# Optimization experiments

Measured on AMD Instinct MI355X. Metric: run time of the kernel, lower is better.

## Reference

```python
import jax, jax.numpy as jnp
import numpy as np

B, C, HIM, WIM = 128, 3, 224, 224
P = 14                      # num_patches per side
PATCH = HIM // P            # 16
IN_D = C * PATCH * PATCH    # 768
D = 256                     # hidden_dim
H = 8                       # num_heads
DH = D // H                 # 32
L = 4                       # num_blocks
OUT = 1000
S = P * P + 1               # 197 tokens incl. class token
EPS = 1e-5


def make_patches(images):
    n, c, h, w = images.shape
    ph, pw = h // P, w // P
    x = images.reshape(n, c, P, ph, P, pw)
    x = x.transpose(0, 2, 4, 1, 3, 5)          # (n, P, P, c, ph, pw)
    return x.reshape(n, P * P, c * ph * pw)


def positional_encodings():
    pos = jnp.arange(S, dtype=jnp.float32)[:, None]
    j = jnp.arange(D)[None, :]
    angle = pos / jnp.power(10000.0, (2 * (j // 2)).astype(jnp.float32) / D)
    return jnp.where(j % 2 == 0, jnp.sin(angle), jnp.cos(angle))  # (S, D)


def layernorm(x, g, b):
    mu = jnp.mean(x, axis=-1, keepdims=True)
    var = jnp.mean(jnp.square(x - mu), axis=-1, keepdims=True)
    return (x - mu) / jnp.sqrt(var + EPS) * g + b


def setup_inputs() -> dict:
    key = jax.random.key(0)
    ks = jax.random.split(key, 32)
    r = lambda k, shp: jax.random.normal(k, shp, jnp.float32) * 0.02
    inp = {
        "images": jax.random.normal(ks[0], (B, C, HIM, WIM), jnp.float32),
        "w_map": r(ks[1], (D, IN_D)), "b_map": r(ks[2], (D,)),
        "cls_tok": jax.random.uniform(ks[3], (1, D), jnp.float32),
        "norm1_g": jnp.ones((L, D)), "norm1_b": jnp.zeros((L, D)),
        "wq": r(ks[4], (L, H, DH, DH)), "bq": r(ks[5], (L, H, DH)),
        "wk": r(ks[6], (L, H, DH, DH)), "bk": r(ks[7], (L, H, DH)),
        "wv": r(ks[8], (L, H, DH, DH)), "bv": r(ks[9], (L, H, DH)),
        "w_last": r(ks[10], (L, D, D)), "b_last": r(ks[11], (L, D)),
        "norm2_g": jnp.ones((L, D)), "norm2_b": jnp.zeros((L, D)),
        "w_mlp1": r(ks[12], (L, 4 * D, D)), "b_mlp1": r(ks[13], (L, 4 * D)),
        "w_mlp2": r(ks[14], (L, D, 4 * D)), "b_mlp2": r(ks[15], (L, D)),
        "w_out": r(ks[16], (OUT, D)), "b_out": r(ks[17], (OUT,)),
    }
    return inp


def reference(images, w_map, b_map, cls_tok, norm1_g, norm1_b,
              wq, bq, wk, bk, wv, bv, w_last, b_last,
              norm2_g, norm2_b, w_mlp1, b_mlp1, w_mlp2, b_mlp2,
              w_out, b_out):
    n = images.shape[0]
    patches = make_patches(images)                         # (n, P*P, IN_D)
    tokens = jnp.einsum('npi,di->npd', patches, w_map) + b_map
    cls = jnp.broadcast_to(cls_tok[None], (n, 1, D))
    out = jnp.concatenate([cls, tokens], axis=1) + positional_encodings()[None]
    scale = 1.0 / jnp.sqrt(jnp.float32(DH))
    for l in range(L):
        x1 = layernorm(out, norm1_g[l], norm1_b[l])
        xh = x1.reshape(n, S, H, DH)
        # per-head Linear: y = x @ W^T + b (torch convention W[out,in])
        q = jnp.einsum('nshd,hed->nshe', xh, wq[l]) + bq[l]
        k = jnp.einsum('nshd,hed->nshe', xh, wk[l]) + bk[l]
        v = jnp.einsum('nshd,hed->nshe', xh, wv[l]) + bv[l]
        attn = jax.nn.softmax(jnp.einsum('nshd,nthd->nhst', q, k) * scale, axis=-1)
        o = jnp.einsum('nhst,nthd->nshd', attn, v).reshape(n, S, D)
        o = jnp.einsum('nsd,ed->nse', o, w_last[l]) + b_last[l]
        out = out + o
        x2 = layernorm(out, norm2_g[l], norm2_b[l])
        h1 = jax.nn.gelu(jnp.einsum('nsd,fd->nsf', x2, w_mlp1[l]) + b_mlp1[l],
                         approximate=False)
        out = out + jnp.einsum('nsf,df->nsd', h1, w_mlp2[l]) + b_mlp2[l]
    cls_out = out[:, 0]                                    # (n, D)
    logits = cls_out @ w_out.T + b_out                     # (n, OUT)
    return jax.nn.softmax(logits, axis=1)
```

## Files before the change

kernel.cpp:

```cpp
#include <hip/hip_runtime.h>
#include <hip/hip_bf16.h>
#include <math.h>


#define SEQ 197
#define DIM 256
#define NB  128
#define MROWS (NB * SEQ)

typedef __attribute__((ext_vector_type(4))) float f32x4;
typedef __attribute__((ext_vector_type(8))) __bf16 bf16x8;
typedef __attribute__((ext_vector_type(8))) short s16x8;

#define GLOAD16(g, l)                                                          \
    __builtin_amdgcn_global_load_lds(                                          \
        (const __attribute__((address_space(1))) void*)(g),                    \
        (__attribute__((address_space(3))) void*)(l), 16, 0, 0)

__device__ __forceinline__ unsigned bf16_rn(float x) {
    union { float f; unsigned u; } c; c.f = x;
    return (c.u + 0x7fffu + ((c.u >> 16) & 1u)) >> 16;
}
__device__ __forceinline__ void split2(float a, unsigned short& hi, unsigned short& lo) {
    unsigned h = bf16_rn(a);
    hi = (unsigned short)h;
    union { unsigned u; float f; } hf; hf.u = h << 16;
    lo = (unsigned short)bf16_rn(a - hf.f);
}
__device__ __forceinline__ int swz(int row, int c) {
    return row * 32 + ((c ^ ((row >> 1) & 3)) << 3);
}

__global__ __launch_bounds__(256) void pe_kernel(float* __restrict__ pe) {
    int s = blockIdx.x, j = threadIdx.x;
    int jh = j >> 1;
    float expo = (float)(2 * jh) * (1.0f / 256.0f);
    float inv_freq = exp2f(-expo * 13.287712379549449f);
    float angle = (float)s * inv_freq;
    pe[s * 256 + j] = (j & 1) ? cosf(angle) : sinf(angle);
}

__global__ __launch_bounds__(256) void embed_cls(const float* __restrict__ cls_tok,
                                                 const float* __restrict__ pe,
                                                 float* __restrict__ out) {
    int n = blockIdx.x, d = threadIdx.x;
    out[(size_t)n * SEQ * DIM + d] = cls_tok[d] + pe[d];
}

__global__ __launch_bounds__(256) void split_weights(const float* __restrict__ src,
                                                     unsigned short* __restrict__ hi,
                                                     unsigned short* __restrict__ lo, int n) {
    for (int i = blockIdx.x * 256 + threadIdx.x; i < n; i += gridDim.x * 256) {
        unsigned short h, l;
        split2(src[i], h, l);
        hi[i] = h; lo[i] = l;
    }
}

__global__ __launch_bounds__(256) void pack_qkv_c(const float* __restrict__ wq,
                                                  const float* __restrict__ wk,
                                                  const float* __restrict__ wv,
                                                  unsigned short* __restrict__ wc) {
    int e = blockIdx.x * 256 + threadIdx.x;
    if (e >= 98304) return;
    int l = e / 24576, r = e % 24576;
    int j = r >> 5, d = r & 31;
    int m = j >> 8, hh = (j >> 5) & 7, ee = j & 31;
    const float* w = (m == 0) ? wq : (m == 1) ? wk : wv;
    wc[e] = (unsigned short)bf16_rn(w[(((size_t)l * 8 + hh) * 32 + ee) * 32 + d]);
}

__global__ __launch_bounds__(256) void pack_qkv_b(const float* __restrict__ bq,
                                                  const float* __restrict__ bk,
                                                  const float* __restrict__ bv,
                                                  float* __restrict__ bp) {
    int e = blockIdx.x * 256 + threadIdx.x;
    if (e >= 3072) return;
    int l = e / 768, j = e % 768;
    int m = j >> 8, jj = j & 255;
    const float* b = (m == 0) ? bq : (m == 1) ? bk : bv;
    bp[e] = b[l * 256 + jj];
}

template <int ACT, int OMODE, bool ALO>
__global__ __launch_bounds__(256) void gemm_as(const unsigned short* __restrict__ Ahi,
                                               const unsigned short* __restrict__ Alo,
                                               const unsigned short* __restrict__ Bhi,
                                               const unsigned short* __restrict__ Blo,
                                               const float* __restrict__ bias,
                                               float* __restrict__ C,
                                               unsigned short* __restrict__ Chi,
                                               unsigned short* __restrict__ Clo,
                                               int M, int N, int K) {
    __shared__ unsigned short Ah[4096], Al[4096], Bh[4096], Bl[4096];
    const int tid = threadIdx.x;
    const int bm = blockIdx.y * 128, bn = blockIdx.x * 128;
    const int lane = tid & 63, wid = tid >> 6;
    const int wm = wid & 1, wn = wid >> 1;
    const int q = lane >> 4, r15 = lane & 15;
    const int rl = lane >> 2, cc = lane & 3;
    const int wr = wid * 32;

    const int row0 = wr + rl, row1 = wr + 16 + rl;
    const int cx0 = (cc ^ ((row0 >> 1) & 3)) << 3;
    const int cx1 = (cc ^ ((row1 >> 1) & 3)) << 3;
    const unsigned short* ah0 = Ahi + (size_t)(bm + row0) * K + cx0;
    const unsigned short* ah1 = Ahi + (size_t)(bm + row1) * K + cx1;
    const unsigned short* al0 = Alo + (size_t)(bm + row0) * K + cx0;
    const unsigned short* al1 = Alo + (size_t)(bm + row1) * K + cx1;
    const unsigned short* bh0 = Bhi + (size_t)(bn + row0) * K + cx0;
    const unsigned short* bh1 = Bhi + (size_t)(bn + row1) * K + cx1;
    const unsigned short* bl0 = Blo + (size_t)(bn + row0) * K + cx0;
    const unsigned short* bl1 = Blo + (size_t)(bn + row1) * K + cx1;

    f32x4 acc[4][4];
#pragma unroll
    for (int i = 0; i < 4; ++i)
#pragma unroll
        for (int j = 0; j < 4; ++j) acc[i][j] = (f32x4){0.f, 0.f, 0.f, 0.f};

    for (int k0 = 0; k0 < K; k0 += 32) {
        GLOAD16(ah0 + k0, &Ah[wr * 32]);
        GLOAD16(ah1 + k0, &Ah[(wr + 16) * 32]);
        if constexpr (ALO) {
            GLOAD16(al0 + k0, &Al[wr * 32]);
            GLOAD16(al1 + k0, &Al[(wr + 16) * 32]);
        }
        GLOAD16(bh0 + k0, &Bh[wr * 32]);
        GLOAD16(bh1 + k0, &Bh[(wr + 16) * 32]);
        GLOAD16(bl0 + k0, &Bl[wr * 32]);
        GLOAD16(bl1 + k0, &Bl[(wr + 16) * 32]);
        __syncthreads();

        s16x8 ah[4], al[4], bhf[4], blf[4];
#pragma unroll
        for (int m = 0; m < 4; ++m) {
            int row = wm * 64 + m * 16 + r15;
            int off = row * 32 + ((q ^ ((row >> 1) & 3)) << 3);
            ah[m] = *(const s16x8*)&Ah[off];
            if constexpr (ALO) al[m] = *(const s16x8*)&Al[off];
        }
#pragma unroll
        for (int n = 0; n < 4; ++n) {
            int row = wn * 64 + n * 16 + r15;
            int off = row * 32 + ((q ^ ((row >> 1) & 3)) << 3);
            bhf[n] = *(const s16x8*)&Bh[off];
            blf[n] = *(const s16x8*)&Bl[off];
        }
#pragma unroll
        for (int m = 0; m < 4; ++m)
#pragma unroll
            for (int n = 0; n < 4; ++n) {
                bf16x8 a_h = __builtin_bit_cast(bf16x8, ah[m]);
                bf16x8 b_h = __builtin_bit_cast(bf16x8, bhf[n]);
                bf16x8 b_l = __builtin_bit_cast(bf16x8, blf[n]);
                acc[m][n] = __builtin_amdgcn_mfma_f32_16x16x32_bf16(a_h, b_h, acc[m][n], 0, 0, 0);
                acc[m][n] = __builtin_amdgcn_mfma_f32_16x16x32_bf16(a_h, b_l, acc[m][n], 0, 0, 0);
                if constexpr (ALO) {
                    bf16x8 a_l = __builtin_bit_cast(bf16x8, al[m]);
                    acc[m][n] = __builtin_amdgcn_mfma_f32_16x16x32_bf16(a_l, b_h, acc[m][n], 0, 0, 0);
                }
            }
        __syncthreads();
    }

#pragma unroll
    for (int n = 0; n < 4; ++n) {
        int col = bn + wn * 64 + n * 16 + r15;
        float bb = bias[col];
#pragma unroll
        for (int m = 0; m < 4; ++m) {
            int r0 = bm + wm * 64 + m * 16 + q * 4;
#pragma unroll
            for (int i = 0; i < 4; ++i) {
                float v = acc[m][n][i] + bb;
                if (ACT == 1) v = 0.5f * v * (1.0f + erff(v * 0.70710678118654752f));
                size_t off = (size_t)(r0 + i) * N + col;
                if constexpr (OMODE == 0) C[off] = v;
                else if constexpr (OMODE == 1) C[off] += v;
                else if constexpr (OMODE == 2) {
                    unsigned short hh, ll; split2(v, hh, ll);
                    Chi[off] = hh; Clo[off] = ll;
                } else {
                    Chi[off] = (unsigned short)bf16_rn(v);
                }
            }
        }
    }
}

__global__ __launch_bounds__(256) void gemm_qkv2(const unsigned short* __restrict__ Ahi,
                                                 const unsigned short* __restrict__ Alo,
                                                 const unsigned short* __restrict__ Bc,
                                                 const float* __restrict__ bias,
                                                 unsigned short* __restrict__ Chi,
                                                 unsigned short* __restrict__ Clo) {
    __shared__ unsigned short Ah[4096], Al[4096], Bh[4096];
    const int tid = threadIdx.x;
    const int bm = blockIdx.y * 128, bn = blockIdx.x * 128;
    const int lane = tid & 63, wid = tid >> 6;
    const int wm = wid & 1, wn = wid >> 1;
    const int q = lane >> 4, r15 = lane & 15;
    const int rl = lane >> 2, cc = lane & 3;
    const int wr = wid * 32;
    const int K = 256, N = 768;

    const int row0 = wr + rl, row1 = wr + 16 + rl;
    const int cx0 = (cc ^ ((row0 >> 1) & 3)) << 3;
    const int cx1 = (cc ^ ((row1 >> 1) & 3)) << 3;
    const unsigned short* ah0 = Ahi + (size_t)(bm + row0) * K + cx0;
    const unsigned short* ah1 = Ahi + (size_t)(bm + row1) * K + cx1;
    const unsigned short* al0 = Alo + (size_t)(bm + row0) * K + cx0;
    const unsigned short* al1 = Alo + (size_t)(bm + row1) * K + cx1;

    const int srow = tid >> 2, sc = tid & 3;
    const int j0 = bn + srow, j1 = bn + srow + 64;
    const int c0 = (j0 >> 5) & 7, c1 = (j1 >> 5) & 7;
    const unsigned short* bc0 = Bc + (size_t)j0 * 32 + sc * 8;
    const unsigned short* bc1 = Bc + (size_t)j1 * 32 + sc * 8;
    const int soff0 = swz(srow, sc), soff1 = swz(srow + 64, sc);

    f32x4 acc[4][4];
#pragma unroll
    for (int i = 0; i < 4; ++i)
#pragma unroll
        for (int j = 0; j < 4; ++j) acc[i][j] = (f32x4){0.f, 0.f, 0.f, 0.f};

    const s16x8 bz = (s16x8){0, 0, 0, 0, 0, 0, 0, 0};
    for (int k0 = 0; k0 < K; k0 += 32) {
        const int kc = k0 >> 5;
        GLOAD16(ah0 + k0, &Ah[wr * 32]);
        GLOAD16(ah1 + k0, &Ah[(wr + 16) * 32]);
        GLOAD16(al0 + k0, &Al[wr * 32]);
        GLOAD16(al1 + k0, &Al[(wr + 16) * 32]);
        *(s16x8*)&Bh[soff0] = (c0 == kc) ? *(const s16x8*)bc0 : bz;
        *(s16x8*)&Bh[soff1] = (c1 == kc) ? *(const s16x8*)bc1 : bz;
        __syncthreads();

        s16x8 ah[4], al[4], bhf[4];
#pragma unroll
        for (int m = 0; m < 4; ++m) {
            int row = wm * 64 + m * 16 + r15;
            int off = row * 32 + ((q ^ ((row >> 1) & 3)) << 3);
            ah[m] = *(const s16x8*)&Ah[off];
            al[m] = *(const s16x8*)&Al[off];
        }
#pragma unroll
        for (int n = 0; n < 4; ++n) {
            int row = wn * 64 + n * 16 + r15;
            int off = row * 32 + ((q ^ ((row >> 1) & 3)) << 3);
            bhf[n] = *(const s16x8*)&Bh[off];
        }
#pragma unroll
        for (int m = 0; m < 4; ++m)
#pragma unroll
            for (int n = 0; n < 4; ++n) {
                bf16x8 a_h = __builtin_bit_cast(bf16x8, ah[m]);
                bf16x8 a_l = __builtin_bit_cast(bf16x8, al[m]);
                bf16x8 b_h = __builtin_bit_cast(bf16x8, bhf[n]);
                acc[m][n] = __builtin_amdgcn_mfma_f32_16x16x32_bf16(a_h, b_h, acc[m][n], 0, 0, 0);
                acc[m][n] = __builtin_amdgcn_mfma_f32_16x16x32_bf16(a_l, b_h, acc[m][n], 0, 0, 0);
            }
        __syncthreads();
    }

#pragma unroll
    for (int n = 0; n < 4; ++n) {
        int col = bn + wn * 64 + n * 16 + r15;
        float bb = bias[col];
#pragma unroll
        for (int m = 0; m < 4; ++m) {
            int r0 = bm + wm * 64 + m * 16 + q * 4;
#pragma unroll
            for (int i = 0; i < 4; ++i) {
                float v = acc[m][n][i] + bb;
                size_t off = (size_t)(r0 + i) * N + col;
                unsigned short hh, ll; split2(v, hh, ll);
                Chi[off] = hh; Clo[off] = ll;
            }
        }
    }
}

__global__ __launch_bounds__(256) void patch_mfma(const float* __restrict__ images,
                                                  const unsigned short* __restrict__ Bhi,
                                                  const unsigned short* __restrict__ Blo,
                                                  const float* __restrict__ b_map,
                                                  const float* __restrict__ pe,
                                                  float* __restrict__ out) {
    __shared__ unsigned short Ah[4096], Al[4096], Bh[4096], Bl[4096];
    const int tid = threadIdx.x;
    const int bm = blockIdx.y * 128, bn = blockIdx.x * 128;
    const int lane = tid & 63, wid = tid >> 6;
    const int wm = wid & 1, wn = wid >> 1;
    const int q = lane >> 4, r15 = lane & 15;
    const int srow = tid >> 2, sc = tid & 3;

    const float* ibase[2];
    {
        int rows[2] = {bm + srow, bm + srow + 64};
#pragma unroll
        for (int t = 0; t < 2; ++t) {
            int n = rows[t] / 196, p = rows[t] % 196;
            ibase[t] = images + (size_t)n * 150528 + (size_t)(p / 14) * 3584 + (p % 14) * 16;
        }
    }
    const int soff0 = swz(srow, sc), soff1 = swz(srow + 64, sc);
    const unsigned short* bh0 = Bhi + (size_t)(bn + srow) * 768 + sc * 8;
    const unsigned short* bl0 = Blo + (size_t)(bn + srow) * 768 + sc * 8;
    const unsigned short* bh1 = Bhi + (size_t)(bn + srow + 64) * 768 + sc * 8;
    const unsigned short* bl1 = Blo + (size_t)(bn + srow + 64) * 768 + sc * 8;

    f32x4 acc[4][4];
#pragma unroll
    for (int i = 0; i < 4; ++i)
#pragma unroll
        for (int j = 0; j < 4; ++j) acc[i][j] = (f32x4){0.f, 0.f, 0.f, 0.f};

    for (int k0 = 0; k0 < 768; k0 += 32) {
        int k = k0 + sc * 8;
        int aoff = (k >> 8) * 50176 + (((k >> 4) & 15)) * 224 + (k & 15);
        {
            float4 v0 = *(const float4*)(ibase[0] + aoff);
            float4 v1 = *(const float4*)(ibase[0] + aoff + 4);
            float vv[8] = {v0.x, v0.y, v0.z, v0.w, v1.x, v1.y, v1.z, v1.w};
            s16x8 hv, lv;
#pragma unroll
            for (int j = 0; j < 8; ++j) {
                unsigned short h, l; split2(vv[j], h, l);
                hv[j] = (short)h; lv[j] = (short)l;
            }
            *(s16x8*)&Ah[soff0] = hv; *(s16x8*)&Al[soff0] = lv;
            v0 = *(const float4*)(ibase[1] + aoff);
            v1 = *(const float4*)(ibase[1] + aoff + 4);
            float ww[8] = {v0.x, v0.y, v0.z, v0.w, v1.x, v1.y, v1.z, v1.w};
#pragma unroll
            for (int j = 0; j < 8; ++j) {
                unsigned short h, l; split2(ww[j], h, l);
                hv[j] = (short)h; lv[j] = (short)l;
            }
            *(s16x8*)&Ah[soff1] = hv; *(s16x8*)&Al[soff1] = lv;
        }
        *(s16x8*)&Bh[soff0] = *(const s16x8*)(bh0 + k0);
        *(s16x8*)&Bl[soff0] = *(const s16x8*)(bl0 + k0);
        *(s16x8*)&Bh[soff1] = *(const s16x8*)(bh1 + k0);
        *(s16x8*)&Bl[soff1] = *(const s16x8*)(bl1 + k0);
        __syncthreads();

        s16x8 ah[4], al[4], bhf[4], blf[4];
#pragma unroll
        for (int m = 0; m < 4; ++m) {
            int row = wm * 64 + m * 16 + r15;
            int off = row * 32 + ((q ^ ((row >> 1) & 3)) << 3);
            ah[m] = *(const s16x8*)&Ah[off];
            al[m] = *(const s16x8*)&Al[off];
        }
#pragma unroll
        for (int n = 0; n < 4; ++n) {
            int row = wn * 64 + n * 16 + r15;
            int off = row * 32 + ((q ^ ((row >> 1) & 3)) << 3);
            bhf[n] = *(const s16x8*)&Bh[off];
            blf[n] = *(const s16x8*)&Bl[off];
        }
#pragma unroll
        for (int m = 0; m < 4; ++m)
#pragma unroll
            for (int n = 0; n < 4; ++n) {
                bf16x8 a_h = __builtin_bit_cast(bf16x8, ah[m]);
                bf16x8 a_l = __builtin_bit_cast(bf16x8, al[m]);
                bf16x8 b_h = __builtin_bit_cast(bf16x8, bhf[n]);
                bf16x8 b_l = __builtin_bit_cast(bf16x8, blf[n]);
                acc[m][n] = __builtin_amdgcn_mfma_f32_16x16x32_bf16(a_h, b_h, acc[m][n], 0, 0, 0);
                acc[m][n] = __builtin_amdgcn_mfma_f32_16x16x32_bf16(a_h, b_l, acc[m][n], 0, 0, 0);
                acc[m][n] = __builtin_amdgcn_mfma_f32_16x16x32_bf16(a_l, b_h, acc[m][n], 0, 0, 0);
            }
        __syncthreads();
    }

#pragma unroll
    for (int n = 0; n < 4; ++n) {
        int col = bn + wn * 64 + n * 16 + r15;
        float bb = b_map[col];
#pragma unroll
        for (int m = 0; m < 4; ++m) {
            int row0 = bm + wm * 64 + m * 16 + q * 4;
#pragma unroll
            for (int i = 0; i < 4; ++i) {
                int rowg = row0 + i;
                int n_img = rowg / 196;
                int p = rowg - n_img * 196;
                out[((size_t)n_img * SEQ + 1 + p) * DIM + col] =
                    acc[m][n][i] + bb + pe[(1 + p) * DIM + col];
            }
        }
    }
}

__global__ __launch_bounds__(256) void attn_mfma2(const unsigned short* __restrict__ qkvh,
                                                  const unsigned short* __restrict__ qkvl,
                                                  unsigned short* __restrict__ oh,
                                                  unsigned short* __restrict__ ol) {
    __shared__ unsigned short Kh[208 * 40];
    __shared__ unsigned short Vt[32 * 232];
    __shared__ unsigned short Pb[4][16 * 232];
    const int tid = threadIdx.x;
    const int lane = tid & 63, wid = tid >> 6;
    const int qh = lane >> 4, qr = lane & 15;
    const int n = blockIdx.x >> 3, h = blockIdx.x & 7;
    const size_t rowbase = (size_t)n * SEQ;
    const float scale = 0.17677669529663687f;

    for (int i = tid; i < 208 * 40 / 2; i += 256) ((uint32_t*)Kh)[i] = 0;
    for (int i = tid; i < 32 * 232 / 2; i += 256) ((uint32_t*)Vt)[i] = 0;
    for (int i = tid; i < 4 * 16 * 232 / 2; i += 256) ((uint32_t*)&Pb[0][0])[i] = 0;
    __syncthreads();

    for (int e = tid; e < SEQ * 4; e += 256) {
        int s = e >> 2, c = e & 3;
        *(s16x8*)&Kh[s * 40 + c * 8] =
            *(const s16x8*)(qkvh + (rowbase + s) * 768 + 256 + h * 32 + c * 8);
    }
    for (int e = tid; e < SEQ * 32; e += 256) {
        int s = e >> 5, d = e & 31;
        Vt[d * 232 + s] = qkvh[(rowbase + s) * 768 + 512 + h * 32 + d];
    }
    __syncthreads();

    unsigned short* Pw = Pb[wid];
    for (int st = wid; st < 13; st += 4) {
        int srow = st * 16 + qr; if (srow > SEQ - 1) srow = SEQ - 1;
        const size_t qoff = (rowbase + srow) * 768 + h * 32 + qh * 8;
        bf16x8 qH = *(const bf16x8*)(qkvh + qoff);
        bf16x8 qL = *(const bf16x8*)(qkvl + qoff);

        f32x4 sacc[13];
#pragma unroll
        for (int tt = 0; tt < 13; ++tt) sacc[tt] = (f32x4){0.f, 0.f, 0.f, 0.f};
#pragma unroll
        for (int tt = 0; tt < 13; ++tt) {
            bf16x8 kf = *(const bf16x8*)&Kh[(tt * 16 + qr) * 40 + qh * 8];
            sacc[tt] = __builtin_amdgcn_mfma_f32_16x16x32_bf16(kf, qH, sacc[tt], 0, 0, 0);
            sacc[tt] = __builtin_amdgcn_mfma_f32_16x16x32_bf16(kf, qL, sacc[tt], 0, 0, 0);
        }
#pragma unroll
        for (int i = 0; i < 4; ++i)
            if (192 + 4 * qh + i > SEQ - 1) sacc[12][i] = -1e4f;
        float mx = -1e4f;
#pragma unroll
        for (int tt = 0; tt < 13; ++tt)
#pragma unroll
            for (int i = 0; i < 4; ++i) mx = fmaxf(mx, sacc[tt][i]);
        mx = fmaxf(mx, __shfl_xor(mx, 16, 64));
        mx = fmaxf(mx, __shfl_xor(mx, 32, 64));
        float sum = 0.f;
#pragma unroll
        for (int tt = 0; tt < 13; ++tt)
#pragma unroll
            for (int i = 0; i < 4; ++i) {
                float p = __expf((sacc[tt][i] - mx) * scale);
                sacc[tt][i] = p; sum += p;
            }
        sum += __shfl_xor(sum, 16, 64);
        sum += __shfl_xor(sum, 32, 64);
        float inv = 1.0f / sum;
#pragma unroll
        for (int tt = 0; tt < 13; ++tt)
#pragma unroll
            for (int i = 0; i < 4; ++i)
                Pw[qr * 232 + tt * 16 + 4 * qh + i] = (unsigned short)bf16_rn(sacc[tt][i]);
#pragma unroll
        for (int i = 0; i < 4; ++i)
            Pw[qr * 232 + 208 + 4 * qh + i] = 0;

        f32x4 oacc[2];
        oacc[0] = (f32x4){0.f, 0.f, 0.f, 0.f};
        oacc[1] = (f32x4){0.f, 0.f, 0.f, 0.f};
#pragma unroll
        for (int kt = 0; kt < 7; ++kt) {
            bf16x8 pf = *(const bf16x8*)&Pw[qr * 232 + kt * 32 + qh * 8];
            bf16x8 v0 = *(const bf16x8*)&Vt[qr * 232 + kt * 32 + qh * 8];
            bf16x8 v1 = *(const bf16x8*)&Vt[(16 + qr) * 232 + kt * 32 + qh * 8];
            oacc[0] = __builtin_amdgcn_mfma_f32_16x16x32_bf16(v0, pf, oacc[0], 0, 0, 0);
            oacc[1] = __builtin_amdgcn_mfma_f32_16x16x32_bf16(v1, pf, oacc[1], 0, 0, 0);
        }
        if (st * 16 + qr < SEQ) {
            size_t obase = (rowbase + st * 16 + qr) * DIM + h * 32;
#pragma unroll
            for (int dt = 0; dt < 2; ++dt)
#pragma unroll
                for (int i = 0; i < 4; ++i) {
                    unsigned short hh, ll;
                    split2(oacc[dt][i] * inv, hh, ll);
                    oh[obase + dt * 16 + 4 * qh + i] = hh;
                    ol[obase + dt * 16 + 4 * qh + i] = ll;
                }
        }
    }
}

__global__ __launch_bounds__(256) void ln_split(const float* __restrict__ x,
                                                unsigned short* __restrict__ yh,
                                                unsigned short* __restrict__ yl,
                                                const float* __restrict__ g,
                                                const float* __restrict__ b) {
    int row = blockIdx.x, tid = threadIdx.x;
    float v = x[(size_t)row * DIM + tid];
    float s = v;
#pragma unroll
    for (int off = 32; off; off >>= 1) s += __shfl_down(s, off, 64);
    __shared__ float red[4];
    if ((tid & 63) == 0) red[tid >> 6] = s;
    __syncthreads();
    float mu = (red[0] + red[1] + red[2] + red[3]) * (1.0f / 256.0f);
    float d = v - mu;
    float s2 = d * d;
#pragma unroll
    for (int off = 32; off; off >>= 1) s2 += __shfl_down(s2, off, 64);
    __shared__ float red2[4];
    if ((tid & 63) == 0) red2[tid >> 6] = s2;
    __syncthreads();
    float var = (red2[0] + red2[1] + red2[2] + red2[3]) * (1.0f / 256.0f);
    float inv_std = 1.0f / sqrtf(var + 1e-5f);
    float y = d * inv_std * g[tid] + b[tid];
    unsigned short hh, ll; split2(y, hh, ll);
    size_t off = (size_t)row * DIM + tid;
    yh[off] = hh; yl[off] = ll;
}

__global__ __launch_bounds__(256) void head_kernel(const float* __restrict__ xin,
                                                   const float* __restrict__ w,
                                                   const float* __restrict__ bias,
                                                   float* __restrict__ res) {
    int n = blockIdx.x, tid = threadIdx.x;
    __shared__ float xs[256];
    xs[tid] = xin[(size_t)n * SEQ * DIM + tid];
    __syncthreads();
    float lg[4];
#pragma unroll
    for (int u = 0; u < 4; ++u) {
        int j = u * 256 + tid;
        float acc = -1e30f;
        if (j < 1000) {
            acc = bias[j];
            for (int kk = 0; kk < 256; kk += 4) {
                float4 wv = *reinterpret_cast<const float4*>(&w[(size_t)j * 256 + kk]);
                acc += xs[kk] * wv.x + xs[kk + 1] * wv.y + xs[kk + 2] * wv.z + xs[kk + 3] * wv.w;
            }
        }
        lg[u] = acc;
    }
    float mx = fmaxf(fmaxf(lg[0], lg[1]), fmaxf(lg[2], lg[3]));
#pragma unroll
    for (int off = 32; off; off >>= 1) mx = fmaxf(mx, __shfl_down(mx, off, 64));
    __shared__ float redm[4];
    if ((tid & 63) == 0) redm[tid >> 6] = mx;
    __syncthreads();
    mx = fmaxf(fmaxf(redm[0], redm[1]), fmaxf(redm[2], redm[3]));
    float e[4], ssum = 0.f;
#pragma unroll
    for (int u = 0; u < 4; ++u) {
        int j = u * 256 + tid;
        e[u] = (j < 1000) ? expf(lg[u] - mx) : 0.f;
        ssum += e[u];
    }
#pragma unroll
    for (int off = 32; off; off >>= 1) ssum += __shfl_down(ssum, off, 64);
    __shared__ float reds[4];
    if ((tid & 63) == 0) reds[tid >> 6] = ssum;
    __syncthreads();
    float inv = 1.0f / (reds[0] + reds[1] + reds[2] + reds[3]);
#pragma unroll
    for (int u = 0; u < 4; ++u) {
        int j = u * 256 + tid;
        if (j < 1000) res[(size_t)n * 1000 + j] = e[u] * inv;
    }
}

extern "C" void kernel_launch(void* const* d_in, const int* in_sizes, int n_in,
                              void* d_out, int out_size, void* d_ws, size_t ws_size,
                              hipStream_t stream) {
    const float* images  = (const float*)d_in[0];
    const float* w_map   = (const float*)d_in[1];
    const float* b_map   = (const float*)d_in[2];
    const float* cls_tok = (const float*)d_in[3];
    const float* norm1_g = (const float*)d_in[4];
    const float* norm1_b = (const float*)d_in[5];
    const float* wq      = (const float*)d_in[6];
    const float* bq      = (const float*)d_in[7];
    const float* wk      = (const float*)d_in[8];
    const float* bk      = (const float*)d_in[9];
    const float* wv      = (const float*)d_in[10];
    const float* bv      = (const float*)d_in[11];
    const float* w_last  = (const float*)d_in[12];
    const float* b_last  = (const float*)d_in[13];
    const float* norm2_g = (const float*)d_in[14];
    const float* norm2_b = (const float*)d_in[15];
    const float* w_mlp1  = (const float*)d_in[16];
    const float* b_mlp1  = (const float*)d_in[17];
    const float* w_mlp2  = (const float*)d_in[18];
    const float* b_mlp2  = (const float*)d_in[19];
    const float* w_out   = (const float*)d_in[20];
    const float* b_out   = (const float*)d_in[21];

    float* wsf = (float*)d_ws;
    const size_t SZ = (size_t)MROWS * DIM;
    float* outb = wsf;
    unsigned short* xh  = (unsigned short*)(wsf + SZ);
    unsigned short* xl  = xh + SZ;
    unsigned short* qkvh = (unsigned short*)(wsf + 2 * SZ);
    unsigned short* qkvl = qkvh + 3 * SZ;
    unsigned short* h1h = (unsigned short*)(wsf + 2 * SZ);
    unsigned short* oh  = (unsigned short*)(wsf + 5 * SZ);
    unsigned short* olo = oh + SZ;
    float* peb  = wsf + 6 * SZ;

    const size_t W_MAP  = 0;
    const size_t W_LAST = 196608;
    const size_t W_MLP1 = 458752;
    const size_t W_MLP2 = 1507328;
    const size_t W_TOTAL = 2555904;
    unsigned short* whi = (unsigned short*)(wsf + 6 * SZ + 50432);
    unsigned short* wlo = whi + W_TOTAL;
    unsigned short* wqkvc = wlo + W_TOTAL;
    float* bqkvp = (float*)(wqkvc + 98304);

    pe_kernel<<<SEQ, 256, 0, stream>>>(peb);
    split_weights<<<768, 256, 0, stream>>>(w_map,  whi + W_MAP,  wlo + W_MAP,  196608);
    split_weights<<<1024, 256, 0, stream>>>(w_last, whi + W_LAST, wlo + W_LAST, 262144);
    split_weights<<<2048, 256, 0, stream>>>(w_mlp1, whi + W_MLP1, wlo + W_MLP1, 1048576);
    split_weights<<<2048, 256, 0, stream>>>(w_mlp2, whi + W_MLP2, wlo + W_MLP2, 1048576);
    pack_qkv_c<<<384, 256, 0, stream>>>(wq, wk, wv, wqkvc);
    pack_qkv_b<<<12, 256, 0, stream>>>(bq, bk, bv, bqkvp);

    embed_cls<<<NB, 256, 0, stream>>>(cls_tok, peb, outb);
    patch_mfma<<<dim3(2, 196), 256, 0, stream>>>(images, whi + W_MAP, wlo + W_MAP,
                                                 b_map, peb, outb);

    for (int l = 0; l < 4; ++l) {
        ln_split<<<MROWS, 256, 0, stream>>>(outb, xh, xl, norm1_g + l * 256, norm1_b + l * 256);
        gemm_qkv2<<<dim3(6, 197), 256, 0, stream>>>(
            xh, xl, wqkvc + (size_t)l * 24576, bqkvp + l * 768, qkvh, qkvl);
        attn_mfma2<<<NB * 8, 256, 0, stream>>>(qkvh, qkvl, oh, olo);
        gemm_as<0, 1, true><<<dim3(2, 197), 256, 0, stream>>>(
            oh, olo, whi + W_LAST + (size_t)l * 65536, wlo + W_LAST + (size_t)l * 65536,
            b_last + l * 256, outb, oh, olo, MROWS, 256, 256);
        ln_split<<<MROWS, 256, 0, stream>>>(outb, xh, xl, norm2_g + l * 256, norm2_b + l * 256);
        gemm_as<1, 3, true><<<dim3(8, 197), 256, 0, stream>>>(
            xh, xl, whi + W_MLP1 + (size_t)l * 262144, wlo + W_MLP1 + (size_t)l * 262144,
            b_mlp1 + l * 1024, outb, h1h, h1h, MROWS, 1024, 256);
        gemm_as<0, 1, false><<<dim3(2, 197), 256, 0, stream>>>(
            h1h, h1h, whi + W_MLP2 + (size_t)l * 262144, wlo + W_MLP2 + (size_t)l * 262144,
            b_mlp2 + l * 256, outb, oh, olo, MROWS, 256, 1024);
    }
    head_kernel<<<NB, 256, 0, stream>>>(outb, w_out, b_out, (float*)d_out);
}
```

Baseline: 1.392 ms.

## Fuse MLP up-projection, GELU and down-projection into one kernel

Replaces the two MLP GEMM launches with a single kernel that computes a 128-row tile of the hidden activation in 128-column chunks. It applies bias and GELU, stores each chunk as bf16 in shared memory, and immediately accumulates its contribution to the output projection. This removes the global write and read of the large 1024-wide hidden tensor. In exchange, only 197 blocks are launched, and each uses large shared memory and many accumulator registers, so GPU occupancy and parallelism drop sharply. The unused split-output modes are also dropped from the generic GEMM.

```diff
diff --git a/kernel.cpp b/kernel.cpp
--- a/kernel.cpp
+++ b/kernel.cpp
@@ -89,8 +89,6 @@
                                                const unsigned short* __restrict__ Blo,
                                                const float* __restrict__ bias,
                                                float* __restrict__ C,
-                                               unsigned short* __restrict__ Chi,
-                                               unsigned short* __restrict__ Clo,
                                                int M, int N, int K) {
     __shared__ unsigned short Ah[4096], Al[4096], Bh[4096], Bl[4096];
     const int tid = threadIdx.x;
@@ -177,14 +175,179 @@
                 if (ACT == 1) v = 0.5f * v * (1.0f + erff(v * 0.70710678118654752f));
                 size_t off = (size_t)(r0 + i) * N + col;
                 if constexpr (OMODE == 0) C[off] = v;
-                else if constexpr (OMODE == 1) C[off] += v;
-                else if constexpr (OMODE == 2) {
-                    unsigned short hh, ll; split2(v, hh, ll);
-                    Chi[off] = hh; Clo[off] = ll;
-                } else {
-                    Chi[off] = (unsigned short)bf16_rn(v);
+                else C[off] += v;
+            }
+        }
+    }
+}
+
+__global__ __launch_bounds__(256) void mlp_fused(const unsigned short* __restrict__ xhp,
+                                                 const unsigned short* __restrict__ xlp,
+                                                 const unsigned short* __restrict__ w1h,
+                                                 const unsigned short* __restrict__ w1l,
+                                                 const float* __restrict__ b1,
+                                                 const unsigned short* __restrict__ w2h,
+                                                 const unsigned short* __restrict__ w2l,
+                                                 const float* __restrict__ b2,
+                                                 float* __restrict__ outb) {
+    __shared__ unsigned short u0[8192];
+    __shared__ unsigned short u1[8192];
+    __shared__ unsigned short Hs[16384];
+    const int tid = threadIdx.x;
+    const int bm = blockIdx.x * 128;
+    const int lane = tid & 63, wid = tid >> 6;
+    const int wm = wid & 1, wn = wid >> 1;
+    const int qh = lane >> 4, r15 = lane & 15;
+    const int rl = lane >> 2, cc = lane & 3;
+    const int wr = wid * 32;
+
+    unsigned short* Xh = u0;      unsigned short* Xl = u0 + 4096;
+    unsigned short* W1h = u1;     unsigned short* W1l = u1 + 4096;
+    unsigned short* W2h = u0;     unsigned short* W2l = u1;
+
+    const int row0 = wr + rl, row1 = wr + 16 + rl;
+    const int cx0 = (cc ^ ((row0 >> 1) & 3)) << 3;
+    const int cx1 = (cc ^ ((row1 >> 1) & 3)) << 3;
+    const unsigned short* xh0 = xhp + (size_t)(bm + row0) * 256 + cx0;
+    const unsigned short* xh1 = xhp + (size_t)(bm + row1) * 256 + cx1;
+    const unsigned short* xl0 = xlp + (size_t)(bm + row0) * 256 + cx0;
+    const unsigned short* xl1 = xlp + (size_t)(bm + row1) * 256 + cx1;
+    const unsigned short* w1h0 = w1h + (size_t)row0 * 256 + cx0;
+    const unsigned short* w1h1 = w1h + (size_t)row1 * 256 + cx1;
+    const unsigned short* w1l0 = w1l + (size_t)row0 * 256 + cx0;
+    const unsigned short* w1l1 = w1l + (size_t)row1 * 256 + cx1;
+
+    const unsigned short* w2hs[4];
+    const unsigned short* w2ls[4];
+#pragma unroll
+    for (int g = 0; g < 4; ++g) {
+        int rowg = wid * 64 + g * 16 + rl;
+        int cxg = (cc ^ ((rowg >> 1) & 3)) << 3;
+        w2hs[g] = w2h + (size_t)rowg * 1024 + cxg;
+        w2ls[g] = w2l + (size_t)rowg * 1024 + cxg;
+    }
+
+    f32x4 oacc[4][8];
+#pragma unroll
+    for (int m = 0; m < 4; ++m)
+#pragma unroll
+        for (int n = 0; n < 8; ++n) oacc[m][n] = (f32x4){0.f, 0.f, 0.f, 0.f};
+
+    for (int j = 0; j < 8; ++j) {
+        const size_t w1off = (size_t)j * 32768;
+        f32x4 hacc[4][4];
+#pragma unroll
+        for (int m = 0; m < 4; ++m)
+#pragma unroll
+            for (int n = 0; n < 4; ++n) hacc[m][n] = (f32x4){0.f, 0.f, 0.f, 0.f};
+
+        for (int k0 = 0; k0 < 256; k0 += 32) {
+            GLOAD16(xh0 + k0, &Xh[wr * 32]);
+            GLOAD16(xh1 + k0, &Xh[(wr + 16) * 32]);
+            GLOAD16(xl0 + k0, &Xl[wr * 32]);
+            GLOAD16(xl1 + k0, &Xl[(wr + 16) * 32]);
+            GLOAD16(w1h0 + w1off + k0, &W1h[wr * 32]);
+            GLOAD16(w1h1 + w1off + k0, &W1h[(wr + 16) * 32]);
+            GLOAD16(w1l0 + w1off + k0, &W1l[wr * 32]);
+            GLOAD16(w1l1 + w1off + k0, &W1l[(wr + 16) * 32]);
+            __syncthreads();
+
+            s16x8 ah[4], al[4], bhf[4], blf[4];
+#pragma unroll
+            for (int m = 0; m < 4; ++m) {
+                int row = wm * 64 + m * 16 + r15;
+                int off = row * 32 + ((qh ^ ((row >> 1) & 3)) << 3);
+                ah[m] = *(const s16x8*)&Xh[off];
+                al[m] = *(const s16x8*)&Xl[off];
+            }
+#pragma unroll
+            for (int n = 0; n < 4; ++n) {
+                int row = wn * 64 + n * 16 + r15;
+                int off = row * 32 + ((qh ^ ((row >> 1) & 3)) << 3);
+                bhf[n] = *(const s16x8*)&W1h[off];
+                blf[n] = *(const s16x8*)&W1l[off];
+            }
+#pragma unroll
+            for (int m = 0; m < 4; ++m)
+#pragma unroll
+                for (int n = 0; n < 4; ++n) {
+                    bf16x8 a_h = __builtin_bit_cast(bf16x8, ah[m]);
+                    bf16x8 a_l = __builtin_bit_cast(bf16x8, al[m]);
+                    bf16x8 b_h = __builtin_bit_cast(bf16x8, bhf[n]);
+                    bf16x8 b_l = __builtin_bit_cast(bf16x8, blf[n]);
+                    hacc[m][n] = __builtin_amdgcn_mfma_f32_16x16x32_bf16(a_h, b_h, hacc[m][n], 0, 0, 0);
+                    hacc[m][n] = __builtin_amdgcn_mfma_f32_16x16x32_bf16(a_h, b_l, hacc[m][n], 0, 0, 0);
+                    hacc[m][n] = __builtin_amdgcn_mfma_f32_16x16x32_bf16(a_l, b_h, hacc[m][n], 0, 0, 0);
                 }
-            }
+            __syncthreads();
+        }
+
+#pragma unroll
+        for (int n = 0; n < 4; ++n) {
+            int col = wn * 64 + n * 16 + r15;
+            float bb = b1[j * 128 + col];
+            int chi = col >> 3, clo = col & 7;
+#pragma unroll
+            for (int m = 0; m < 4; ++m) {
+                int rbase = wm * 64 + m * 16 + qh * 4;
+#pragma unroll
+                for (int i = 0; i < 4; ++i) {
+                    int row = rbase + i;
+                    float v = hacc[m][n][i] + bb;
+                    v = 0.5f * v * (1.0f + erff(v * 0.70710678118654752f));
+                    Hs[row * 128 + ((chi ^ (row & 7)) << 3) + clo] =
+                        (unsigned short)bf16_rn(v);
+                }
+            }
+        }
+        __syncthreads();
+
+        for (int kk = 0; kk < 4; ++kk) {
+#pragma unroll
+            for (int g = 0; g < 4; ++g) {
+                GLOAD16(w2hs[g] + j * 128 + kk * 32, &W2h[(wid * 64 + g * 16) * 32]);
+                GLOAD16(w2ls[g] + j * 128 + kk * 32, &W2l[(wid * 64 + g * 16) * 32]);
+            }
+            __syncthreads();
+
+            s16x8 pa[4], pbh[8], pbl[8];
+#pragma unroll
+            for (int m = 0; m < 4; ++m) {
+                int row = wm * 64 + m * 16 + r15;
+                int c = kk * 4 + qh;
+                pa[m] = *(const s16x8*)&Hs[row * 128 + ((c ^ (row & 7)) << 3)];
+            }
+#pragma unroll
+            for (int n = 0; n < 8; ++n) {
+                int row = wn * 128 + n * 16 + r15;
+                int off = row * 32 + ((qh ^ ((row >> 1) & 3)) << 3);
+                pbh[n] = *(const s16x8*)&W2h[off];
+                pbl[n] = *(const s16x8*)&W2l[off];
+            }
+#pragma unroll
+            for (int m = 0; m < 4; ++m)
+#pragma unroll
+                for (int n = 0; n < 8; ++n) {
+                    bf16x8 a_h = __builtin_bit_cast(bf16x8, pa[m]);
+                    bf16x8 b_h = __builtin_bit_cast(bf16x8, pbh[n]);
+                    bf16x8 b_l = __builtin_bit_cast(bf16x8, pbl[n]);
+                    oacc[m][n] = __builtin_amdgcn_mfma_f32_16x16x32_bf16(a_h, b_h, oacc[m][n], 0, 0, 0);
+                    oacc[m][n] = __builtin_amdgcn_mfma_f32_16x16x32_bf16(a_h, b_l, oacc[m][n], 0, 0, 0);
+                }
+            __syncthreads();
+        }
+    }
+
+#pragma unroll
+    for (int n = 0; n < 8; ++n) {
+        int col = wn * 128 + n * 16 + r15;
+        float bb = b2[col];
+#pragma unroll
+        for (int m = 0; m < 4; ++m) {
+            int r0 = bm + wm * 64 + m * 16 + qh * 4;
+#pragma unroll
+            for (int i = 0; i < 4; ++i)
+                outb[(size_t)(r0 + i) * 256 + col] += oacc[m][n][i] + bb;
         }
     }
 }
@@ -609,7 +772,6 @@
     unsigned short* xl  = xh + SZ;
     unsigned short* qkvh = (unsigned short*)(wsf + 2 * SZ);
     unsigned short* qkvl = qkvh + 3 * SZ;
-    unsigned short* h1h = (unsigned short*)(wsf + 2 * SZ);
     unsigned short* oh  = (unsigned short*)(wsf + 5 * SZ);
     unsigned short* olo = oh + SZ;
     float* peb  = wsf + 6 * SZ;
@@ -643,14 +805,13 @@
         attn_mfma2<<<NB * 8, 256, 0, stream>>>(qkvh, qkvl, oh, olo);
         gemm_as<0, 1, true><<<dim3(2, 197), 256, 0, stream>>>(
             oh, olo, whi + W_LAST + (size_t)l * 65536, wlo + W_LAST + (size_t)l * 65536,
-            b_last + l * 256, outb, oh, olo, MROWS, 256, 256);
+            b_last + l * 256, outb, MROWS, 256, 256);
         ln_split<<<MROWS, 256, 0, stream>>>(outb, xh, xl, norm2_g + l * 256, norm2_b + l * 256);
-        gemm_as<1, 3, true><<<dim3(8, 197), 256, 0, stream>>>(
+        mlp_fused<<<197, 256, 0, stream>>>(
             xh, xl, whi + W_MLP1 + (size_t)l * 262144, wlo + W_MLP1 + (size_t)l * 262144,
-            b_mlp1 + l * 1024, outb, h1h, h1h, MROWS, 1024, 256);
-        gemm_as<0, 1, false><<<dim3(2, 197), 256, 0, stream>>>(
-            h1h, h1h, whi + W_MLP2 + (size_t)l * 262144, wlo + W_MLP2 + (size_t)l * 262144,
-            b_mlp2 + l * 256, outb, oh, olo, MROWS, 256, 1024);
+            b_mlp1 + l * 1024,
+            whi + W_MLP2 + (size_t)l * 262144, wlo + W_MLP2 + (size_t)l * 262144,
+            b_mlp2 + l * 256, outb);
     }
     head_kernel<<<NB, 256, 0, stream>>>(outb, w_out, b_out, (float*)d_out);
 }
```

Result: slower. 1.557 ms (+11.8%).
